# Optimization experiments

Measured on AMD Instinct MI355X. Metric: run time of the kernel, lower is better.

## Reference

```python
import jax, jax.numpy as jnp
import numpy as np

B, N, C, H = 8, 1024, 768, 12
D = C // H  # 64


def setup_inputs() -> dict:
    key = jax.random.key(0)
    ks = jax.random.split(key, 6)
    x = jax.random.normal(ks[0], (B, N, C), dtype=jnp.float32)
    pad_mask = jnp.ones((B, N), dtype=jnp.int32)
    # params (torch Linear stored transposed; here kept as (in, out) for x @ W)
    s = 1.0 / np.sqrt(C)
    w_attn = jax.random.uniform(ks[1], (C, 3 * C), jnp.float32, -s, s)
    b_attn = jax.random.uniform(ks[2], (3 * C,), jnp.float32, -s, s)
    w_proj = jax.random.uniform(ks[3], (C, C), jnp.float32, -s, s)
    b_proj = jax.random.uniform(ks[4], (C,), jnp.float32, -s, s)
    return {"x": x, "pad_mask": pad_mask, "w_attn": w_attn,
            "b_attn": b_attn, "w_proj": w_proj, "b_proj": b_proj}


def reference(x, pad_mask, w_attn, b_attn, w_proj, b_proj):
    # qkv projection
    qkv = x @ w_attn + b_attn                      # [B,N,3C]
    q, k, v = jnp.split(qkv, 3, axis=-1)
    q = q.reshape(B, N, H, D).transpose(0, 2, 1, 3)  # [B,H,N,D]
    k = k.reshape(B, N, H, D).transpose(0, 2, 1, 3)
    v = v.reshape(B, N, H, D).transpose(0, 2, 1, 3)
    scale = 1.0 / np.sqrt(D)
    att = jnp.einsum('bhqd,bhkd->bhqk', q, k) * scale  # [B,H,N,N]
    # NOTE: original code's causal masked_fill is non-in-place and discarded,
    # so the causal mask is NOT applied. Only the pad mask (over query rows) is.
    pm = pad_mask.reshape(B, 1, N, 1)
    att = jnp.where(pm == 0, -jnp.inf, att)
    att = jax.nn.softmax(att, axis=-1)
    out = jnp.einsum('bhqk,bhkd->bhqd', att, v)     # [B,H,N,D]
    out = out.transpose(0, 2, 1, 3).reshape(B, N, C)
    # dropout layers are identity in eval mode
    return out @ w_proj + b_proj
```

## Files before the change

### kernel.cpp

```cpp
#include <hip/hip_runtime.h>
#include <hip/hip_bf16.h>

#define B_  8
#define N_  1024
#define C_  768
#define H_  12
#define D_  64
#define C3  2304
#define C2  1536

typedef unsigned short ushort_t;
typedef __attribute__((ext_vector_type(8))) short bf16x8;
typedef __attribute__((ext_vector_type(4))) float f32x4;

__device__ __forceinline__ float bf2f(ushort_t u) {
    union { unsigned int i; float f; } v;
    v.i = ((unsigned int)u) << 16;
    return v.f;
}

__device__ __forceinline__ ushort_t f2bf(float f) {
    union { float f; unsigned int i; } v;
    v.f = f;
    unsigned int x = v.i;
    if ((x & 0x7f800000u) == 0x7f800000u && (x & 0x007fffffu))
        return (ushort_t)((x >> 16) | 0x0040u);
    return (ushort_t)((x + 0x7fffu + ((x >> 16) & 1u)) >> 16);
}

__device__ __forceinline__ void st1(float* p, float v) { *p = v; }
__device__ __forceinline__ void st1(ushort_t* p, float v) { *p = f2bf(v); }

__global__ __launch_bounds__(256) void cvt_bf16(
    const float* __restrict__ X, ushort_t* __restrict__ Y, int n)
{
    int i = (blockIdx.x * 256 + threadIdx.x) * 4;
    if (i < n) {
        float4 f = *reinterpret_cast<const float4*>(X + i);
        ushort4 o;
        o.x = f2bf(f.x); o.y = f2bf(f.y); o.z = f2bf(f.z); o.w = f2bf(f.w);
        *reinterpret_cast<ushort4*>(Y + i) = o;
    }
}

__global__ __launch_bounds__(256) void transpose_to_bf16(
    const float* __restrict__ W, ushort_t* __restrict__ WT, int K, int Nn)
{
    __shared__ float t[32][33];
    const int n0 = blockIdx.x * 32, k0 = blockIdx.y * 32;
    const int tx = threadIdx.x & 31, ty = threadIdx.x >> 5;
    #pragma unroll
    for (int i = 0; i < 4; ++i) {
        const int k = ty + i * 8;
        t[k][tx] = W[(size_t)(k0 + k) * Nn + n0 + tx];
    }
    __syncthreads();
    #pragma unroll
    for (int i = 0; i < 4; ++i) {
        const int n = ty + i * 8;
        WT[(size_t)(n0 + n) * K + k0 + tx] = f2bf(t[tx][n]);
    }
}

#define GBK 64

__device__ __forceinline__ void gld_lds16(const ushort_t* g, ushort_t* lds) {
    __builtin_amdgcn_global_load_lds(
        (const __attribute__((address_space(1))) void*)g,
        (__attribute__((address_space(3))) void*)lds, 16, 0, 0);
}

template<typename TO, bool SCALEQ>
__global__ __launch_bounds__(256) void gemm_mfma(
    const ushort_t* __restrict__ A, const ushort_t* __restrict__ BT,
    const float* __restrict__ bias, TO* __restrict__ Y, int ldY,
    ushort_t* __restrict__ vtOut, int M, int K, int Nn)
{
    __shared__ ushort_t As[128 * GBK];
    __shared__ ushort_t Bs[128 * GBK];

    const int tid  = threadIdx.x;
    const int wave = tid >> 6;
    const int lane = tid & 63;
    const int row0 = blockIdx.y * 128;
    const int col0 = blockIdx.x * 128;
    const int wr   = (wave >> 1) * 64;
    const int wc   = (wave & 1) * 64;
    const int l15  = lane & 15;
    const int quad = lane >> 4;
    const int l7   = l15 & 7;

    const int srow = lane >> 3;
    const int sg   = (lane & 7) ^ srow;

    f32x4 acc[4][4] = {};

    for (int k0 = 0; k0 < K; k0 += GBK) {
        __syncthreads();
        #pragma unroll
        for (int it = 0; it < 4; ++it) {
            const int baseRow = wave * 32 + it * 8;
            const int r = baseRow + srow;
            gld_lds16(&A [(size_t)(row0 + r) * K + k0 + sg * 8], &As[baseRow * GBK]);
            gld_lds16(&BT[(size_t)(col0 + r) * K + k0 + sg * 8], &Bs[baseRow * GBK]);
        }
        __syncthreads();

        #pragma unroll
        for (int kc = 0; kc < 2; ++kc) {
            bf16x8 af[4], bf[4];
            #pragma unroll
            for (int i = 0; i < 4; ++i) {
                const int aslot = (kc * 4 + quad) ^ l7;
                af[i] = *reinterpret_cast<const bf16x8*>(
                    &As[(wr + i * 16 + l15) * GBK + aslot * 8]);
                bf[i] = *reinterpret_cast<const bf16x8*>(
                    &Bs[(wc + i * 16 + l15) * GBK + aslot * 8]);
            }
            #pragma unroll
            for (int i = 0; i < 4; ++i)
                #pragma unroll
                for (int j = 0; j < 4; ++j)
                    acc[i][j] = __builtin_amdgcn_mfma_f32_16x16x32_bf16(
                        af[i], bf[j], acc[i][j], 0, 0, 0);
        }
    }

    const float qs = (SCALEQ && (col0 + wc) < C_) ? 0.125f : 1.0f;

    if (vtOut != nullptr && col0 >= C2) {
        #pragma unroll
        for (int i = 0; i < 4; ++i) {
            const int r0 = row0 + wr + i * 16 + quad * 4;
            const int bb = r0 >> 10;
            const int n  = r0 & 1023;
            #pragma unroll
            for (int j = 0; j < 4; ++j) {
                const int c  = col0 + wc + j * 16 + l15;
                const int cv = c - C2;
                const int hh = cv >> 6, d = cv & 63;
                const float bv = bias[c];
                ushort4 o;
                o.x = f2bf(acc[i][j][0] + bv);
                o.y = f2bf(acc[i][j][1] + bv);
                o.z = f2bf(acc[i][j][2] + bv);
                o.w = f2bf(acc[i][j][3] + bv);
                *reinterpret_cast<ushort4*>(
                    &vtOut[((size_t)(bb * H_ + hh) * D_ + d) * N_ + n]) = o;
            }
        }
    } else {
        #pragma unroll
        for (int i = 0; i < 4; ++i) {
            const int r = row0 + wr + i * 16 + quad * 4;
            #pragma unroll
            for (int j = 0; j < 4; ++j) {
                const int c = col0 + wc + j * 16 + l15;
                const float bv = bias[c];
                #pragma unroll
                for (int t = 0; t < 4; ++t)
                    st1(&Y[(size_t)(r + t) * ldY + c], (acc[i][j][t] + bv) * qs);
            }
        }
    }
}

#define LDT 72

__global__ __launch_bounds__(256) void attn_mfma(
    const ushort_t* __restrict__ qk, const ushort_t* __restrict__ vt,
    const int* __restrict__ pad_mask, ushort_t* __restrict__ y)
{
    __shared__ ushort_t Ks [64 * LDT];
    __shared__ ushort_t Vts[64 * LDT];
    __shared__ ushort_t Ps [4][32 * LDT];

    const int tid  = threadIdx.x;
    const int wave = tid >> 6;
    const int lane = tid & 63;
    const int l15  = lane & 15;
    const int quad = lane >> 4;

    const int qt = blockIdx.x & 7;
    const int h  = (blockIdx.x >> 3) % H_;
    const int b  = blockIdx.x / (8 * H_);
    const int q0 = qt * 128 + wave * 32;

    const ushort_t* qkB = qk + (size_t)b * N_ * C2;
    const ushort_t* vtB = vt + ((size_t)(b * H_ + h)) * D_ * N_;
    const int ho = h * D_;

    bf16x8 qf[2][2];
    #pragma unroll
    for (int rt = 0; rt < 2; ++rt)
        #pragma unroll
        for (int kc = 0; kc < 2; ++kc)
            qf[rt][kc] = *reinterpret_cast<const bf16x8*>(
                &qkB[(size_t)(q0 + rt * 16 + l15) * C2 + ho + kc * 32 + quad * 8]);

    int mrow[2][4];
    #pragma unroll
    for (int rt = 0; rt < 2; ++rt)
        #pragma unroll
        for (int t = 0; t < 4; ++t)
            mrow[rt][t] = pad_mask[b * N_ + q0 + rt * 16 + quad * 4 + t];

    f32x4 oacc[2][4] = {};
    float den[2][4] = {};

    const int srow = tid >> 3;
    const int scol = (tid & 7) * 8;

    for (int k0 = 0; k0 < N_; k0 += 64) {
        __syncthreads();
        #pragma unroll
        for (int half = 0; half < 2; ++half) {
            const int r = srow + half * 32;
            uint4 kv = *reinterpret_cast<const uint4*>(
                &qkB[(size_t)(k0 + r) * C2 + C_ + ho + scol]);
            uint4 vv = *reinterpret_cast<const uint4*>(
                &vtB[(size_t)r * N_ + k0 + scol]);
            *reinterpret_cast<uint4*>(&Ks [r * LDT + scol]) = kv;
            *reinterpret_cast<uint4*>(&Vts[r * LDT + scol]) = vv;
        }
        __syncthreads();

        f32x4 s[2][4] = {};
        #pragma unroll
        for (int kc = 0; kc < 2; ++kc) {
            bf16x8 kf[4];
            #pragma unroll
            for (int ct = 0; ct < 4; ++ct)
                kf[ct] = *reinterpret_cast<const bf16x8*>(
                    &Ks[(ct * 16 + l15) * LDT + kc * 32 + quad * 8]);
            #pragma unroll
            for (int rt = 0; rt < 2; ++rt)
                #pragma unroll
                for (int ct = 0; ct < 4; ++ct)
                    s[rt][ct] = __builtin_amdgcn_mfma_f32_16x16x32_bf16(
                        qf[rt][kc], kf[ct], s[rt][ct], 0, 0, 0);
        }

        ushort_t* Pw = Ps[wave];
        #pragma unroll
        for (int rt = 0; rt < 2; ++rt)
            #pragma unroll
            for (int ct = 0; ct < 4; ++ct)
                #pragma unroll
                for (int t = 0; t < 4; ++t) {
                    float p = __expf(s[rt][ct][t]);
                    unsigned u = (__float_as_uint(p) + 0x8000u) & 0xffff0000u;
                    den[rt][t] += __uint_as_float(u);
                    Pw[(rt * 16 + quad * 4 + t) * LDT + ct * 16 + l15] =
                        (ushort_t)(u >> 16);
                }

        #pragma unroll
        for (int kc = 0; kc < 2; ++kc) {
            bf16x8 pf[2], vf[4];
            #pragma unroll
            for (int rt = 0; rt < 2; ++rt)
                pf[rt] = *reinterpret_cast<const bf16x8*>(
                    &Pw[(rt * 16 + l15) * LDT + kc * 32 + quad * 8]);
            #pragma unroll
            for (int dt = 0; dt < 4; ++dt)
                vf[dt] = *reinterpret_cast<const bf16x8*>(
                    &Vts[(dt * 16 + l15) * LDT + kc * 32 + quad * 8]);
            #pragma unroll
            for (int rt = 0; rt < 2; ++rt)
                #pragma unroll
                for (int dt = 0; dt < 4; ++dt)
                    oacc[rt][dt] = __builtin_amdgcn_mfma_f32_16x16x32_bf16(
                        pf[rt], vf[dt], oacc[rt][dt], 0, 0, 0);
        }
    }

    ushort_t* Pw = Ps[wave];
    #pragma unroll
    for (int rt = 0; rt < 2; ++rt)
        #pragma unroll
        for (int t = 0; t < 4; ++t) {
            float v = den[rt][t];
            v += __shfl_xor(v, 1);
            v += __shfl_xor(v, 2);
            v += __shfl_xor(v, 4);
            v += __shfl_xor(v, 8);
            const float inv = mrow[rt][t] ? 1.0f / v : __builtin_nanf("");
            const int row = rt * 16 + quad * 4 + t;
            #pragma unroll
            for (int dt = 0; dt < 4; ++dt)
                Pw[row * LDT + dt * 16 + l15] = f2bf(oacc[rt][dt][t] * inv);
        }
    {
        const int orow = lane >> 1;
        const int ocol = (lane & 1) * 32;
        const size_t gr = (size_t)(b * N_ + q0 + orow) * C_ + ho + ocol;
        #pragma unroll
        for (int i2 = 0; i2 < 4; ++i2) {
            uint4 w = *reinterpret_cast<const uint4*>(&Pw[orow * LDT + ocol + i2 * 8]);
            *reinterpret_cast<uint4*>(&y[gr + i2 * 8]) = w;
        }
    }
}

extern "C" void kernel_launch(void* const* d_in, const int* in_sizes, int n_in,
                              void* d_out, int out_size, void* d_ws, size_t ws_size,
                              hipStream_t stream)
{
    const float* x      = (const float*)d_in[0];
    const int*   pad    = (const int*)d_in[1];
    const float* w_attn = (const float*)d_in[2];
    const float* b_attn = (const float*)d_in[3];
    const float* w_proj = (const float*)d_in[4];
    const float* b_proj = (const float*)d_in[5];
    float* out = (float*)d_out;

    ushort_t* qkb = (ushort_t*)d_ws;
    ushort_t* vtb = qkb + (size_t)B_ * N_ * C2;
    ushort_t* y   = vtb + (size_t)B_ * H_ * D_ * N_;
    ushort_t* xb  = y;
    ushort_t* wat = y + (size_t)B_ * N_ * C_;
    ushort_t* wpt = wat + (size_t)C3 * C_;

    const int M = B_ * N_;

    cvt_bf16<<<dim3((M * C_) / (256 * 4)), dim3(256), 0, stream>>>(x, xb, M * C_);
    transpose_to_bf16<<<dim3(C3 / 32, C_ / 32), dim3(256), 0, stream>>>(
        w_attn, wat, C_, C3);
    transpose_to_bf16<<<dim3(C_ / 32, C_ / 32), dim3(256), 0, stream>>>(
        w_proj, wpt, C_, C_);

    gemm_mfma<ushort_t, true><<<dim3(C3 / 128, M / 128), dim3(256), 0, stream>>>(
        xb, wat, b_attn, qkb, C2, vtb, M, C_, C3);

    attn_mfma<<<dim3(B_ * H_ * 8), dim3(256), 0, stream>>>(qkb, vtb, pad, y);

    gemm_mfma<float, false><<<dim3(C_ / 128, M / 128), dim3(256), 0, stream>>>(
        y, wpt, b_proj, out, C_, nullptr, M, C_, C_);
}
```

Measured before the change: 205.2 us.

## Keep attention probabilities in registers, prefetch K/V tiles, use exp2 with folded log2e

The score MFMA now computes the transposed product, so each lane holds the P values it needs as the A operand of the PV MFMA. This removes the per-wave LDS round trip for P, and V is read with a matching permuted k ordering. The log2(e) factor is folded into the Q scale so the exponent uses the native exp2. K/V tiles for the next step are loaded into registers while the current tile is computed. The changes add register pressure and rely on the permuted k ordering being consistent between P and V.

```diff
diff --git a/kernel.cpp b/kernel.cpp
--- a/kernel.cpp
+++ b/kernel.cpp
@@ -12,6 +12,8 @@
 typedef unsigned short ushort_t;
 typedef __attribute__((ext_vector_type(8))) short bf16x8;
 typedef __attribute__((ext_vector_type(4))) float f32x4;
+typedef __attribute__((ext_vector_type(4))) unsigned int u32x4;
+typedef __attribute__((ext_vector_type(2))) unsigned int u32x2;
 
 __device__ __forceinline__ float bf2f(ushort_t u) {
     union { unsigned int i; float f; } v;
@@ -126,7 +128,7 @@
         }
     }
 
-    const float qs = (SCALEQ && (col0 + wc) < C_) ? 0.125f : 1.0f;
+    const float qs = (SCALEQ && (col0 + wc) < C_) ? 0.1803368801f : 1.0f;
 
     if (vtOut != nullptr && col0 >= C2) {
         #pragma unroll
@@ -171,9 +173,9 @@
     const ushort_t* __restrict__ qk, const ushort_t* __restrict__ vt,
     const int* __restrict__ pad_mask, ushort_t* __restrict__ y)
 {
-    __shared__ ushort_t Ks [64 * LDT];
-    __shared__ ushort_t Vts[64 * LDT];
-    __shared__ ushort_t Ps [4][32 * LDT];
+    __shared__ ushort_t KV[2 * 64 * LDT];
+    ushort_t* const Ks  = KV;
+    ushort_t* const Vts = KV + 64 * LDT;
 
     const int tid  = threadIdx.x;
     const int wave = tid >> 6;
@@ -206,24 +208,39 @@
             mrow[rt][t] = pad_mask[b * N_ + q0 + rt * 16 + quad * 4 + t];
 
     f32x4 oacc[2][4] = {};
-    float den[2][4] = {};
+    float den[2] = {};
 
     const int srow = tid >> 3;
     const int scol = (tid & 7) * 8;
 
+    uint4 kvr[2], vvr[2];
+    #pragma unroll
+    for (int hf = 0; hf < 2; ++hf) {
+        const int r = srow + hf * 32;
+        kvr[hf] = *reinterpret_cast<const uint4*>(
+            &qkB[(size_t)r * C2 + C_ + ho + scol]);
+        vvr[hf] = *reinterpret_cast<const uint4*>(&vtB[(size_t)r * N_ + scol]);
+    }
+
     for (int k0 = 0; k0 < N_; k0 += 64) {
         __syncthreads();
         #pragma unroll
-        for (int half = 0; half < 2; ++half) {
-            const int r = srow + half * 32;
-            uint4 kv = *reinterpret_cast<const uint4*>(
-                &qkB[(size_t)(k0 + r) * C2 + C_ + ho + scol]);
-            uint4 vv = *reinterpret_cast<const uint4*>(
-                &vtB[(size_t)r * N_ + k0 + scol]);
-            *reinterpret_cast<uint4*>(&Ks [r * LDT + scol]) = kv;
-            *reinterpret_cast<uint4*>(&Vts[r * LDT + scol]) = vv;
+        for (int hf = 0; hf < 2; ++hf) {
+            const int r = srow + hf * 32;
+            *reinterpret_cast<uint4*>(&Ks [r * LDT + scol]) = kvr[hf];
+            *reinterpret_cast<uint4*>(&Vts[r * LDT + scol]) = vvr[hf];
         }
         __syncthreads();
+        if (k0 + 64 < N_) {
+            #pragma unroll
+            for (int hf = 0; hf < 2; ++hf) {
+                const int r = srow + hf * 32;
+                kvr[hf] = *reinterpret_cast<const uint4*>(
+                    &qkB[(size_t)(k0 + 64 + r) * C2 + C_ + ho + scol]);
+                vvr[hf] = *reinterpret_cast<const uint4*>(
+                    &vtB[(size_t)r * N_ + k0 + 64 + scol]);
+            }
+        }
 
         f32x4 s[2][4] = {};
         #pragma unroll
@@ -238,58 +255,78 @@
                 #pragma unroll
                 for (int ct = 0; ct < 4; ++ct)
                     s[rt][ct] = __builtin_amdgcn_mfma_f32_16x16x32_bf16(
-                        qf[rt][kc], kf[ct], s[rt][ct], 0, 0, 0);
-        }
-
-        ushort_t* Pw = Ps[wave];
+                        kf[ct], qf[rt][kc], s[rt][ct], 0, 0, 0);
+        }
+
+        unsigned pk[2][4][2];
         #pragma unroll
         for (int rt = 0; rt < 2; ++rt)
             #pragma unroll
-            for (int ct = 0; ct < 4; ++ct)
+            for (int ct = 0; ct < 4; ++ct) {
+                const unsigned x0 = __float_as_uint(
+                    __builtin_amdgcn_exp2f(s[rt][ct][0])) + 0x8000u;
+                const unsigned x1 = __float_as_uint(
+                    __builtin_amdgcn_exp2f(s[rt][ct][1])) + 0x8000u;
+                const unsigned x2 = __float_as_uint(
+                    __builtin_amdgcn_exp2f(s[rt][ct][2])) + 0x8000u;
+                const unsigned x3 = __float_as_uint(
+                    __builtin_amdgcn_exp2f(s[rt][ct][3])) + 0x8000u;
+                const unsigned c0 = (x0 >> 16) | (x1 & 0xffff0000u);
+                const unsigned c1 = (x2 >> 16) | (x3 & 0xffff0000u);
+                den[rt] += __uint_as_float(c0 << 16)
+                         + __uint_as_float(c0 & 0xffff0000u)
+                         + __uint_as_float(c1 << 16)
+                         + __uint_as_float(c1 & 0xffff0000u);
+                pk[rt][ct][0] = c0;
+                pk[rt][ct][1] = c1;
+            }
+
+        #pragma unroll
+        for (int kc = 0; kc < 2; ++kc) {
+            bf16x8 pf[2];
+            #pragma unroll
+            for (int rt = 0; rt < 2; ++rt) {
+                union { u32x4 u; bf16x8 b; } pu;
+                pu.u = (u32x4){pk[rt][kc * 2][0], pk[rt][kc * 2][1],
+                               pk[rt][kc * 2 + 1][0], pk[rt][kc * 2 + 1][1]};
+                pf[rt] = pu.b;
+            }
+            #pragma unroll
+            for (int dt = 0; dt < 4; ++dt) {
+                union { u32x2 u2[2]; bf16x8 b; } vu;
+                const ushort_t* vrow =
+                    &Vts[(dt * 16 + l15) * LDT + kc * 32 + quad * 4];
+                vu.u2[0] = *reinterpret_cast<const u32x2*>(vrow);
+                vu.u2[1] = *reinterpret_cast<const u32x2*>(vrow + 16);
+                const bf16x8 vf = vu.b;
                 #pragma unroll
-                for (int t = 0; t < 4; ++t) {
-                    float p = __expf(s[rt][ct][t]);
-                    unsigned u = (__float_as_uint(p) + 0x8000u) & 0xffff0000u;
-                    den[rt][t] += __uint_as_float(u);
-                    Pw[(rt * 16 + quad * 4 + t) * LDT + ct * 16 + l15] =
-                        (ushort_t)(u >> 16);
-                }
-
-        #pragma unroll
-        for (int kc = 0; kc < 2; ++kc) {
-            bf16x8 pf[2], vf[4];
-            #pragma unroll
-            for (int rt = 0; rt < 2; ++rt)
-                pf[rt] = *reinterpret_cast<const bf16x8*>(
-                    &Pw[(rt * 16 + l15) * LDT + kc * 32 + quad * 8]);
+                for (int rt = 0; rt < 2; ++rt)
+                    oacc[rt][dt] = __builtin_amdgcn_mfma_f32_16x16x32_bf16(
+                        pf[rt], vf, oacc[rt][dt], 0, 0, 0);
+            }
+        }
+    }
+
+    __syncthreads();
+    ushort_t* const scratch = KV + wave * 32 * LDT;
+
+    #pragma unroll
+    for (int rt = 0; rt < 2; ++rt) {
+        float v = den[rt];
+        v += __shfl_xor(v, 16);
+        v += __shfl_xor(v, 32);
+        den[rt] = v;
+    }
+    #pragma unroll
+    for (int rt = 0; rt < 2; ++rt)
+        #pragma unroll
+        for (int t = 0; t < 4; ++t) {
+            const float dv  = __shfl(den[rt], quad * 4 + t);
+            const float inv = mrow[rt][t] ? 1.0f / dv : __builtin_nanf("");
+            const int row = rt * 16 + quad * 4 + t;
             #pragma unroll
             for (int dt = 0; dt < 4; ++dt)
-                vf[dt] = *reinterpret_cast<const bf16x8*>(
-                    &Vts[(dt * 16 + l15) * LDT + kc * 32 + quad * 8]);
-            #pragma unroll
-            for (int rt = 0; rt < 2; ++rt)
-                #pragma unroll
-                for (int dt = 0; dt < 4; ++dt)
-                    oacc[rt][dt] = __builtin_amdgcn_mfma_f32_16x16x32_bf16(
-                        pf[rt], vf[dt], oacc[rt][dt], 0, 0, 0);
-        }
-    }
-
-    ushort_t* Pw = Ps[wave];
-    #pragma unroll
-    for (int rt = 0; rt < 2; ++rt)
-        #pragma unroll
-        for (int t = 0; t < 4; ++t) {
-            float v = den[rt][t];
-            v += __shfl_xor(v, 1);
-            v += __shfl_xor(v, 2);
-            v += __shfl_xor(v, 4);
-            v += __shfl_xor(v, 8);
-            const float inv = mrow[rt][t] ? 1.0f / v : __builtin_nanf("");
-            const int row = rt * 16 + quad * 4 + t;
-            #pragma unroll
-            for (int dt = 0; dt < 4; ++dt)
-                Pw[row * LDT + dt * 16 + l15] = f2bf(oacc[rt][dt][t] * inv);
+                scratch[row * LDT + dt * 16 + l15] = f2bf(oacc[rt][dt][t] * inv);
         }
     {
         const int orow = lane >> 1;
@@ -297,7 +334,8 @@
         const size_t gr = (size_t)(b * N_ + q0 + orow) * C_ + ho + ocol;
         #pragma unroll
         for (int i2 = 0; i2 < 4; ++i2) {
-            uint4 w = *reinterpret_cast<const uint4*>(&Pw[orow * LDT + ocol + i2 * 8]);
+            uint4 w = *reinterpret_cast<const uint4*>(
+                &scratch[orow * LDT + ocol + i2 * 8]);
             *reinterpret_cast<uint4*>(&y[gr + i2 * 8]) = w;
         }
     }
```

Measured after the change: 223.7 us. 1.09x slower.
